# Kernel tuning notes

Measured on AMD Instinct MI355X. Metric: run time of the kernel, lower is better.

## Reference

```python
import jax, jax.numpy as jnp
import numpy as np

N, E, G = 100000, 1600000, 8
IN, H, OUT = 3, 64, 20


def setup_inputs() -> dict:
    key = jax.random.key(0)
    ks = jax.random.split(key, 24)
    def nrm(k, shape, scale=0.1):
        return jax.random.normal(k, shape, dtype=jnp.float32) * scale
    inp = {}
    inp["x"] = jax.random.normal(ks[0], (N, IN), dtype=jnp.float32)
    inp["edge_index"] = jax.random.randint(ks[1], (2, E), 0, N, dtype=jnp.int32)
    inp["batch"] = jnp.sort(jax.random.randint(ks[2], (N,), 0, G, dtype=jnp.int32))
    dims = [(IN, H), (H, H), (H, H)]  # 3 GATConv layers (initial + layers-1)
    for i, (di, do) in enumerate(dims):
        inp[f"W{i}"] = nrm(ks[3 + 4 * i], (di, do))
        inp[f"as{i}"] = nrm(ks[4 + 4 * i], (do,))
        inp[f"ad{i}"] = nrm(ks[5 + 4 * i], (do,))
        inp[f"b{i}"] = jnp.zeros((do,), jnp.float32)
    inp["vn_emb0"] = jnp.zeros((1, H), jnp.float32)  # constant-0 init per module
    inp["m1_w1"] = nrm(ks[15], (H, H)); inp["m1_b1"] = jnp.zeros((H,), jnp.float32)
    inp["m1_w2"] = nrm(ks[16], (H, H)); inp["m1_b2"] = jnp.zeros((H,), jnp.float32)
    inp["mf_w1"] = nrm(ks[17], (H, H)); inp["mf_b1"] = jnp.zeros((H,), jnp.float32)
    inp["mf_w2"] = nrm(ks[18], (H, OUT)); inp["mf_b2"] = jnp.zeros((OUT,), jnp.float32)
    inp["out_w"] = nrm(ks[19], (H, OUT)); inp["out_b"] = jnp.zeros((OUT,), jnp.float32)
    return inp


def _gat(x, src, dst, W, a_s, a_d, b):
    # PyG GATConv, 1 head: h = xW; e_ij = LeakyReLU_0.2(a_s.h_j + a_d.h_i);
    # alpha = softmax over incoming edges of each dst node; out_i = sum_j alpha_ij h_j + b
    h = x @ W                                                  # [N, H]
    lg = jax.nn.leaky_relu((h @ a_s)[src] + (h @ a_d)[dst], 0.2)  # [E+N]
    m = jax.ops.segment_max(lg, dst, num_segments=N)
    m = jnp.where(jnp.isfinite(m), m, 0.0)
    p = jnp.exp(lg - m[dst])
    denom = jax.ops.segment_sum(p, dst, num_segments=N)
    alpha = p / denom[dst]
    return jax.ops.segment_sum(alpha[:, None] * h[src], dst, num_segments=N) + b


def _forward(x, edge_index, batch, params):
    (W0, as0, ad0, b0, W1, as1, ad1, b1, W2, as2, ad2, b2,
     vn_emb0, m1_w1, m1_b1, m1_w2, m1_b2, mf_w1, mf_b1, mf_w2, mf_b2,
     out_w, out_b) = params
    loops = jnp.arange(N, dtype=edge_index.dtype)  # GATConv add_self_loops=True
    src = jnp.concatenate([edge_index[0], loops])
    dst = jnp.concatenate([edge_index[1], loops])
    act = lambda v: jax.nn.leaky_relu(v, 0.01)  # nn.LeakyReLU default slope
    h = act(_gat(x, src, dst, W0, as0, ad0, b0))
    h = act(_gat(h, src, dst, W1, as1, ad1, b1))
    h = act(_gat(h, src, dst, W2, as2, ad2, b2))
    # virtual node: global_add_pool(out, batch) + Embedding(0) (zero-init)
    vn = jax.ops.segment_sum(h, batch, num_segments=G) + vn_emb0[0]
    vn = jax.nn.relu(vn @ m1_w1 + m1_b1)
    vn = jax.nn.relu(vn @ m1_w2 + m1_b2)
    vn = jax.nn.relu(vn @ mf_w1 + mf_b1)
    vn = jax.nn.relu(vn @ mf_w2 + mf_b2)
    return (h @ out_w + out_b, vn)


def reference(x, edge_index, batch, W0, as0, ad0, b0, W1, as1, ad1, b1,
              W2, as2, ad2, b2, vn_emb0, m1_w1, m1_b1, m1_w2, m1_b2,
              mf_w1, mf_b1, mf_w2, mf_b2, out_w, out_b):
    params = (W0, as0, ad0, b0, W1, as1, ad1, b1, W2, as2, ad2, b2,
              vn_emb0, m1_w1, m1_b1, m1_w2, m1_b2, mf_w1, mf_b1, mf_w2, mf_b2,
              out_w, out_b)
    return _forward(x, edge_index, batch, params)
```

## Files before the change

### kernel.cpp

```cpp
#include <hip/hip_runtime.h>
#include <hip/hip_bf16.h>

#define H 64
#define OUTD 20
#define NGRAPH 8
#define CAP 64
#define NB 128

typedef __attribute__((ext_vector_type(8))) short bf16x8;
typedef __attribute__((ext_vector_type(4))) float f32x4;
typedef __attribute__((ext_vector_type(8))) unsigned short u16x8;

__device__ __forceinline__ float ldp(const void* p, int i, bool f32) {
    return f32 ? ((const float*)p)[i]
               : __bfloat162float(((const __hip_bfloat16*)p)[i]);
}

__device__ __forceinline__ float bfu(unsigned short u) {
    union { unsigned int i; float f; } c; c.i = ((unsigned)u) << 16; return c.f;
}
__device__ __forceinline__ unsigned short fbits(float f) {
    __hip_bfloat16 b = __float2bfloat16(f);
    return *reinterpret_cast<unsigned short*>(&b);
}

__global__ void detect_dtype(const unsigned short* __restrict__ xb, int n_u16,
                             int* __restrict__ flag) {
    __shared__ int sh[256];
    int t = threadIdx.x;
    int m = min(n_u16, 4096);
    int bad = 0;
    for (int i = t; i < m; i += 256) {
        unsigned e = (xb[i] >> 7) & 0xFF;
        bad += (e >= 0x90) ? 1 : 0;
    }
    sh[t] = bad;
    __syncthreads();
    for (int off = 128; off; off >>= 1) {
        if (t < off) sh[t] += sh[t + off];
        __syncthreads();
    }
    if (t == 0) *flag = (sh[0] > (m >> 4)) ? 1 : 0;
}


__global__ void bucketA_dense0(const int* __restrict__ dst, int* __restrict__ bcnt,
                               int E, int n, int nA, int EPC,
                               const void* __restrict__ x, const void* __restrict__ W,
                               const void* __restrict__ a_s, const void* __restrict__ a_d,
                               __hip_bfloat16* __restrict__ h, float* __restrict__ s,
                               float* __restrict__ d, const int* __restrict__ flagp) {
    if ((int)blockIdx.x < nA) {
        __shared__ unsigned acnt[NB];
        int t = threadIdx.x;
        for (int i = t; i < NB; i += 256) acnt[i] = 0;
        __syncthreads();
        int base = blockIdx.x * (256 * EPC) + t;
        for (int i = 0; i < EPC; ++i) {
            int e = base + i * 256;
            if (e < E) {
                int dn = dst[e];
                if ((unsigned)dn < (unsigned)n) atomicAdd(&acnt[dn >> 10], 1u);
            }
        }
        __syncthreads();
        for (int i = t; i < NB; i += 256) bcnt[blockIdx.x * NB + i] = acnt[i];
        return;
    }
    const bool f32 = (*flagp != 0);
    int idx = ((int)blockIdx.x - nA) * 256 + threadIdx.x;
    int node = idx >> 6;
    int f = idx & 63;
    if (node >= n) return;
    float acc = 0.f;
    for (int k = 0; k < 3; ++k)
        acc += ldp(x, node * 3 + k, f32) * ldp(W, k * H + f, f32);
    h[(size_t)node * H + f] = __float2bfloat16(acc);
    float sv = acc * ldp(a_s, f, f32);
    float dv = acc * ldp(a_d, f, f32);
    for (int off = 32; off; off >>= 1) {
        sv += __shfl_xor(sv, off);
        dv += __shfl_xor(dv, off);
    }
    if (f == 0) { s[node] = sv; d[node] = dv; }
}

__global__ void bucketB1(const int* __restrict__ bcnt, int* __restrict__ boff,
                         int* __restrict__ btot, int nA) {
    __shared__ int sh[256];
    int b = blockIdx.x, t = threadIdx.x;
    int v = (t < nA) ? bcnt[t * NB + b] : 0;
    sh[t] = v;
    __syncthreads();
    for (int off = 1; off < 256; off <<= 1) {
        int add = (t >= off) ? sh[t - off] : 0;
        __syncthreads();
        sh[t] += add;
        __syncthreads();
    }
    if (t < nA) boff[t * NB + b] = sh[t] - v;
    if (t == 255) btot[b] = sh[255];
}

__global__ void bucketB2(const int* __restrict__ btot, int* __restrict__ bstart) {
    __shared__ int sh[NB];
    int t = threadIdx.x;
    int v = btot[t];
    sh[t] = v;
    __syncthreads();
    for (int off = 1; off < NB; off <<= 1) {
        int add = (t >= off) ? sh[t - off] : 0;
        __syncthreads();
        sh[t] += add;
        __syncthreads();
    }
    bstart[t] = sh[t] - v;
    if (t == NB - 1) bstart[NB] = sh[NB - 1];
}

__global__ void bucketC(const int* __restrict__ src, const int* __restrict__ dst,
                        const int* __restrict__ boff, const int* __restrict__ bstart,
                        unsigned* __restrict__ ebuf, int E, int n, int EPC) {
    __shared__ int base[NB];
    __shared__ unsigned lcur[NB];
    int t = threadIdx.x;
    for (int i = t; i < NB; i += 256) {
        base[i] = bstart[i] + boff[blockIdx.x * NB + i];
        lcur[i] = 0;
    }
    __syncthreads();
    int eb = blockIdx.x * (256 * EPC) + t;
    for (int i = 0; i < EPC; ++i) {
        int e = eb + i * 256;
        if (e < E) {
            int dn = dst[e];
            if ((unsigned)dn < (unsigned)n) {
                int b = dn >> 10;
                unsigned pos = atomicAdd(&lcur[b], 1u);
                ebuf[base[b] + pos] = ((unsigned)src[e] << 10) | (unsigned)(dn & 1023);
            }
        }
    }
}

__global__ __launch_bounds__(1024) void bucketD(const unsigned* __restrict__ ebuf,
                                                const int* __restrict__ bstart,
                                                int* __restrict__ cnt,
                                                int* __restrict__ col, int n) {
    __shared__ unsigned lcnt[1024];
    int b = blockIdx.x, t = threadIdx.x;
    lcnt[t] = 0;
    __syncthreads();
    int beg = bstart[b], end = bstart[b + 1];
    for (int i = beg + t; i < end; i += 1024) {
        unsigned e = ebuf[i];
        int loc = (int)(e & 1023u);
        int sn = (int)(e >> 10);
        unsigned pos = atomicAdd(&lcnt[loc], 1u);
        if (pos < CAP) col[(size_t)((b << 10) + loc) * CAP + pos] = sn;
    }
    __syncthreads();
    int node = (b << 10) + t;
    if (node < n) cnt[node] = (int)min(lcnt[t], (unsigned)CAP);
}


__global__ __launch_bounds__(256) void denseN_mfma(
    const __hip_bfloat16* __restrict__ in,
    const void* __restrict__ W,
    const void* __restrict__ a_s, const void* __restrict__ a_d,
    __hip_bfloat16* __restrict__ h, float* __restrict__ s,
    float* __restrict__ d, int n, const int* __restrict__ flagp) {
    const bool f32 = (*flagp != 0);
    __shared__ short Wt[64 * 72];
    int t = threadIdx.x;
    for (int i = t; i < 4096; i += 256) {
        int k = i >> 6, nf = i & 63;
        Wt[nf * 72 + k] = (short)fbits(ldp(W, i, f32));
    }
    __syncthreads();

    int wid = t >> 6, lane = t & 63;
    int quad = lane >> 4, n16 = lane & 15;
    int nodeBase = blockIdx.x * 64 + wid * 16;
    int mrow = nodeBase + n16;
    int mclamp = min(mrow, n - 1);
    const short* inp = (const short*)in;
    const short* arow = inp + (size_t)mclamp * 64;
    bf16x8 a0 = *(const bf16x8*)(arow + quad * 8);
    bf16x8 a1 = *(const bf16x8*)(arow + 32 + quad * 8);

    float as_v[4], ad_v[4];
    for (int nt = 0; nt < 4; ++nt) {
        as_v[nt] = ldp(a_s, nt * 16 + n16, f32);
        ad_v[nt] = ldp(a_d, nt * 16 + n16, f32);
    }

    float sv[4] = {0.f, 0.f, 0.f, 0.f}, dv[4] = {0.f, 0.f, 0.f, 0.f};
    f32x4 accs[4];
    for (int nt = 0; nt < 4; ++nt) {
        const short* wrow = Wt + (nt * 16 + n16) * 72;
        bf16x8 b0 = *(const bf16x8*)(wrow + quad * 8);
        bf16x8 b1 = *(const bf16x8*)(wrow + 32 + quad * 8);
        f32x4 c = {0.f, 0.f, 0.f, 0.f};
        c = __builtin_amdgcn_mfma_f32_16x16x32_bf16(a0, b0, c, 0, 0, 0);
        c = __builtin_amdgcn_mfma_f32_16x16x32_bf16(a1, b1, c, 0, 0, 0);
        accs[nt] = c;
        for (int r = 0; r < 4; ++r) {
            sv[r] += c[r] * as_v[nt];
            dv[r] += c[r] * ad_v[nt];
        }
    }

    for (int r = 0; r < 4; ++r) {
        int node = nodeBase + quad * 4 + r;
        if (node < n) {
            __hip_bfloat16* hr = h + (size_t)node * 64;
            for (int nt = 0; nt < 4; ++nt)
                hr[nt * 16 + n16] = __float2bfloat16(accs[nt][r]);
        }
    }
    for (int r = 0; r < 4; ++r) {
        for (int mask = 1; mask < 16; mask <<= 1) {
            sv[r] += __shfl_xor(sv[r], mask);
            dv[r] += __shfl_xor(dv[r], mask);
        }
    }
    if (n16 == 0) {
        for (int r = 0; r < 4; ++r) {
            int node = nodeBase + quad * 4 + r;
            if (node < n) { s[node] = sv[r]; d[node] = dv[r]; }
        }
    }
}


__global__ void gat_aggregate(const __hip_bfloat16* __restrict__ h,
                              const float* __restrict__ s, const float* __restrict__ d,
                              const int* __restrict__ cnt, const int* __restrict__ col,
                              const void* __restrict__ bias,
                              __hip_bfloat16* __restrict__ out, int n,
                              const int* __restrict__ flagp) {
    const bool f32 = (*flagp != 0);
    int node = (blockIdx.x * blockDim.x + threadIdx.x) >> 6;
    if (node >= n) return;
    int lane = threadIdx.x & 63;
    int deg = min(cnt[node], CAP);
    int D = deg + 1;
    size_t base = (size_t)node * CAP;
    float di = d[node];

    if (D <= 64) {
        bool act = lane < D;
        int j = (lane < deg) ? col[base + lane] : node;
        j = ((unsigned)j < (unsigned)n) ? j : 0;
        float v = act ? s[j] + di : -INFINITY;
        v = v > 0.f ? v : 0.2f * v;
        float m = v;
        for (int off = 32; off; off >>= 1) m = fmaxf(m, __shfl_xor(m, off));
        float wgt = act ? __expf(v - m) : 0.f;
        float wsum = wgt;
        for (int off = 32; off; off >>= 1) wsum += __shfl_xor(wsum, off);

        const u16x8* h8 = (const u16x8*)h;
        int c = lane & 7, q = lane >> 3;
        float a[8] = {0.f, 0.f, 0.f, 0.f, 0.f, 0.f, 0.f, 0.f};
        int groups = (D + 7) >> 3;
        for (int p = 0; p < groups; ++p) {
            int t = 8 * p + q;
            float wt = __shfl(wgt, t);
            int jt = __shfl(j, t);
            u16x8 hv = h8[jt * 8 + c];
            a[0] += wt * bfu(hv[0]);
            a[1] += wt * bfu(hv[1]);
            a[2] += wt * bfu(hv[2]);
            a[3] += wt * bfu(hv[3]);
            a[4] += wt * bfu(hv[4]);
            a[5] += wt * bfu(hv[5]);
            a[6] += wt * bfu(hv[6]);
            a[7] += wt * bfu(hv[7]);
        }
        for (int i = 0; i < 8; ++i) {
            a[i] += __shfl_xor(a[i], 8);
            a[i] += __shfl_xor(a[i], 16);
            a[i] += __shfl_xor(a[i], 32);
        }
        if (lane < 8) {
            float inv = 1.f / fmaxf(wsum, 1e-20f);
            u16x8 ov;
            for (int i = 0; i < 8; ++i) {
                float o = a[i] * inv + ldp(bias, 8 * c + i, f32);
                o = o > 0.f ? o : 0.01f * o;
                ov[i] = fbits(o);
            }
            ((u16x8*)out)[(size_t)node * 8 + c] = ov;
        }
        return;
    }

    float m = -INFINITY;
    for (int e = lane; e < D; e += 64) {
        int j = (e < deg) ? col[base + e] : node;
        j = ((unsigned)j < (unsigned)n) ? j : 0;
        float v = s[j] + di;
        v = v > 0.f ? v : 0.2f * v;
        m = fmaxf(m, v);
    }
    for (int off = 32; off; off >>= 1) m = fmaxf(m, __shfl_xor(m, off));
    if (!(m > -INFINITY)) m = 0.f;

    float acc = 0.f, wsum = 0.f;
    for (int b = 0; b < D; b += 64) {
        int e = b + lane;
        float w = 0.f;
        int j = 0;
        if (e < D) {
            j = (e < deg) ? col[base + e] : node;
            j = ((unsigned)j < (unsigned)n) ? j : 0;
            float v = s[j] + di;
            v = v > 0.f ? v : 0.2f * v;
            w = __expf(v - m);
        }
        wsum += w;
        int c2 = min(64, D - b);
        for (int t = 0; t < c2; ++t) {
            float wt = __shfl(w, t);
            int jt = __shfl(j, t);
            acc += wt * __bfloat162float(h[(size_t)jt * H + lane]);
        }
    }
    for (int off = 32; off; off >>= 1) wsum += __shfl_xor(wsum, off);

    float o = acc / fmaxf(wsum, 1e-20f) + ldp(bias, lane, f32);
    o = o > 0.f ? o : 0.01f * o;
    out[(size_t)node * H + lane] = __float2bfloat16(o);
}


__global__ __launch_bounds__(256) void proj_pool(
    const __hip_bfloat16* __restrict__ h,
    const void* __restrict__ W, const void* __restrict__ b,
    void* __restrict__ out, int n, const int* __restrict__ flagp,
    int projBlocks, const int* __restrict__ batch, float* __restrict__ vn) {
    const bool f32 = (*flagp != 0);
    if ((int)blockIdx.x < projBlocks) {
        __shared__ short Wt[32 * 72];
        int t = threadIdx.x;
        for (int i = t; i < 32 * 64; i += 256) {
            int o = i >> 6, k = i & 63;
            Wt[o * 72 + k] = (o < OUTD) ? (short)fbits(ldp(W, k * OUTD + o, f32)) : 0;
        }
        __syncthreads();

        int wid = t >> 6, lane = t & 63;
        int quad = lane >> 4, n16 = lane & 15;
        int nodeBase = blockIdx.x * 64 + wid * 16;
        int mclamp = min(nodeBase + n16, n - 1);
        const short* arow = (const short*)h + (size_t)mclamp * 64;
        bf16x8 a0 = *(const bf16x8*)(arow + quad * 8);
        bf16x8 a1 = *(const bf16x8*)(arow + 32 + quad * 8);

        f32x4 acc0 = {0.f, 0.f, 0.f, 0.f}, acc1 = {0.f, 0.f, 0.f, 0.f};
        {
            const short* wrow = Wt + n16 * 72;
            bf16x8 b0 = *(const bf16x8*)(wrow + quad * 8);
            bf16x8 b1 = *(const bf16x8*)(wrow + 32 + quad * 8);
            acc0 = __builtin_amdgcn_mfma_f32_16x16x32_bf16(a0, b0, acc0, 0, 0, 0);
            acc0 = __builtin_amdgcn_mfma_f32_16x16x32_bf16(a1, b1, acc0, 0, 0, 0);
        }
        {
            const short* wrow = Wt + (16 + n16) * 72;
            bf16x8 b0 = *(const bf16x8*)(wrow + quad * 8);
            bf16x8 b1 = *(const bf16x8*)(wrow + 32 + quad * 8);
            acc1 = __builtin_amdgcn_mfma_f32_16x16x32_bf16(a0, b0, acc1, 0, 0, 0);
            acc1 = __builtin_amdgcn_mfma_f32_16x16x32_bf16(a1, b1, acc1, 0, 0, 0);
        }
        float bv0 = ldp(b, n16, f32);
        float bv1 = (n16 < OUTD - 16) ? ldp(b, 16 + n16, f32) : 0.f;
        for (int r = 0; r < 4; ++r) {
            int node = nodeBase + quad * 4 + r;
            if (node >= n) break;
            float o0 = acc0[r] + bv0;
            if (f32) ((float*)out)[node * OUTD + n16] = o0;
            else     ((__hip_bfloat16*)out)[node * OUTD + n16] = __float2bfloat16(o0);
            if (n16 < OUTD - 16) {
                float o1 = acc1[r] + bv1;
                if (f32) ((float*)out)[node * OUTD + 16 + n16] = o1;
                else     ((__hip_bfloat16*)out)[node * OUTD + 16 + n16] = __float2bfloat16(o1);
            }
        }
        return;
    }
    __shared__ float part[NGRAPH * H];
    int t = threadIdx.x;
    for (int i = t; i < NGRAPH * H; i += 256) part[i] = 0.f;
    __syncthreads();
    int pb = (int)blockIdx.x - projBlocks;
    int npb = gridDim.x - projBlocks;
    int wid = t >> 6, lane = t & 63;
    int gwave = pb * 4 + wid;
    int nwaves = npb * 4;
    int chunk = (n + nwaves - 1) / nwaves;
    int beg = gwave * chunk;
    int end = min(n, beg + chunk);
    if (beg < end) {
        float acc = 0.f;
        int cur = batch[beg];
        for (int i = beg; i < end; ++i) {
            int g = batch[i];
            if (g != cur) {
                if ((unsigned)cur < NGRAPH) atomicAdd(&part[cur * H + lane], acc);
                acc = 0.f;
                cur = g;
            }
            acc += __bfloat162float(h[(size_t)i * H + lane]);
        }
        if ((unsigned)cur < NGRAPH) atomicAdd(&part[cur * H + lane], acc);
    }
    __syncthreads();
    for (int i = t; i < NGRAPH * H; i += 256) {
        float v = part[i];
        if (v != 0.f) atomicAdd(&vn[i], v);
    }
}


__global__ void vn_mlp(const float* __restrict__ vn, const void* __restrict__ emb,
                       const void* __restrict__ w1, const void* __restrict__ b1,
                       const void* __restrict__ w2, const void* __restrict__ b2,
                       const void* __restrict__ w3, const void* __restrict__ b3,
                       const void* __restrict__ w4, const void* __restrict__ b4,
                       void* __restrict__ out, int out1_off, const int* __restrict__ flagp) {
    const bool f32 = (*flagp != 0);
    __shared__ float A[NGRAPH * H], B[NGRAPH * H];
    int t = threadIdx.x;
    int g = t >> 6, f = t & 63;
    A[t] = vn[t] + ldp(emb, f, f32);
    __syncthreads();
    float acc = ldp(b1, f, f32);
    for (int k = 0; k < H; ++k) acc += A[g * H + k] * ldp(w1, k * H + f, f32);
    B[t] = fmaxf(acc, 0.f);
    __syncthreads();
    acc = ldp(b2, f, f32);
    for (int k = 0; k < H; ++k) acc += B[g * H + k] * ldp(w2, k * H + f, f32);
    A[t] = fmaxf(acc, 0.f);
    __syncthreads();
    acc = ldp(b3, f, f32);
    for (int k = 0; k < H; ++k) acc += A[g * H + k] * ldp(w3, k * H + f, f32);
    B[t] = fmaxf(acc, 0.f);
    __syncthreads();
    if (f < OUTD) {
        acc = ldp(b4, f, f32);
        for (int k = 0; k < H; ++k) acc += B[g * H + k] * ldp(w4, k * OUTD + f, f32);
        acc = fmaxf(acc, 0.f);
        int idx = out1_off + g * OUTD + f;
        if (f32) ((float*)out)[idx] = acc;
        else     ((__hip_bfloat16*)out)[idx] = __float2bfloat16(acc);
    }
}


extern "C" void kernel_launch(void* const* d_in, const int* in_sizes, int n_in,
                              void* d_out, int out_size, void* d_ws, size_t ws_size,
                              hipStream_t stream) {
    const void* x   = d_in[0];
    const int* ei   = (const int*)d_in[1];
    const int* batch= (const int*)d_in[2];
    const void* W0  = d_in[3];
    const void* as0 = d_in[4];
    const void* ad0 = d_in[5];
    const void* b0  = d_in[6];
    const void* W1  = d_in[7];
    const void* as1 = d_in[8];
    const void* ad1 = d_in[9];
    const void* b1  = d_in[10];
    const void* W2  = d_in[11];
    const void* as2 = d_in[12];
    const void* ad2 = d_in[13];
    const void* b2  = d_in[14];
    const void* vne = d_in[15];
    const void* m1w1 = d_in[16];
    const void* m1b1 = d_in[17];
    const void* m1w2 = d_in[18];
    const void* m1b2 = d_in[19];
    const void* mfw1 = d_in[20];
    const void* mfb1 = d_in[21];
    const void* mfw2 = d_in[22];
    const void* mfb2 = d_in[23];
    const void* outw = d_in[24];
    const void* outb = d_in[25];

    const int N = in_sizes[2];
    const int E = in_sizes[1] / 2;
    const int* srcp = ei;
    const int* dstp = ei + E;

    char* w = (char*)d_ws;
    auto alloc = [&](size_t bytes) -> void* {
        void* p = (void*)w;
        w += ((bytes + 255) / 256) * 256;
        return p;
    };
    int*   flag   = (int*)alloc(256);
    int*   bcnt   = (int*)alloc((size_t)256 * NB * 4);
    int*   boff   = (int*)alloc((size_t)256 * NB * 4);
    int*   btot   = (int*)alloc((size_t)NB * 4);
    int*   bstart = (int*)alloc((size_t)(NB + 1) * 4);
    unsigned* ebuf= (unsigned*)alloc((size_t)E * 4);
    int*   cnt    = (int*)alloc((size_t)N * 4);
    int*   col    = (int*)alloc((size_t)N * CAP * 4);
    __hip_bfloat16* featA = (__hip_bfloat16*)alloc((size_t)N * H * 2);
    __hip_bfloat16* featB = (__hip_bfloat16*)alloc((size_t)N * H * 2);
    __hip_bfloat16* hbuf  = (__hip_bfloat16*)alloc((size_t)N * H * 2);
    float* sArr   = (float*)alloc((size_t)N * 4);
    float* dArr   = (float*)alloc((size_t)N * 4);
    float* vn     = (float*)alloc((size_t)NGRAPH * H * 4);

    const int nbN64 = (N * H + 255) / 256;
    const int nb64 = (N + 63) / 64;
    const int projBlocks = (N + 63) / 64;
    int EPC = 32;
    int nA = (E + 256 * EPC - 1) / (256 * EPC);
    while (nA > 256) { EPC <<= 1; nA = (E + 256 * EPC - 1) / (256 * EPC); }

    detect_dtype<<<1, 256, 0, stream>>>((const unsigned short*)x, in_sizes[0], flag);

    hipMemsetAsync(vn, 0, (size_t)NGRAPH * H * 4, stream);
    bucketA_dense0<<<nA + nbN64, 256, 0, stream>>>(
        dstp, bcnt, E, N, nA, EPC, x, W0, as0, ad0, hbuf, sArr, dArr, flag);
    bucketB1<<<NB, 256, 0, stream>>>(bcnt, boff, btot, nA);
    bucketB2<<<1, NB, 0, stream>>>(btot, bstart);
    bucketC<<<nA, 256, 0, stream>>>(srcp, dstp, boff, bstart, ebuf, E, N, EPC);
    bucketD<<<NB, 1024, 0, stream>>>(ebuf, bstart, cnt, col, N);

    gat_aggregate<<<nbN64, 256, 0, stream>>>(hbuf, sArr, dArr, cnt, col, b0, featA, N, flag);
    denseN_mfma<<<nb64, 256, 0, stream>>>(featA, W1, as1, ad1, hbuf, sArr, dArr, N, flag);
    gat_aggregate<<<nbN64, 256, 0, stream>>>(hbuf, sArr, dArr, cnt, col, b1, featB, N, flag);
    denseN_mfma<<<nb64, 256, 0, stream>>>(featB, W2, as2, ad2, hbuf, sArr, dArr, N, flag);
    gat_aggregate<<<nbN64, 256, 0, stream>>>(hbuf, sArr, dArr, cnt, col, b2, featA, N, flag);

    proj_pool<<<projBlocks + 512, 256, 0, stream>>>(featA, outw, outb, d_out, N, flag,
                                                    projBlocks, batch, vn);
    vn_mlp<<<1, 512, 0, stream>>>(vn, vne, m1w1, m1b1, m1w2, m1b2, mfw1, mfb1, mfw2, mfb2,
                                  d_out, N * OUTD, flag);
}
```

Measured before the change: 440.0 us.

## Fuse GAT aggregation with next-layer dense projection and final proj/pool

Each GAT layer's neighbor aggregation now writes its 64 node rows into LDS, and the same block then runs the MFMA projection for the next layer, or the output projection plus graph pooling for the last layer. This removes the global write and re-read of the intermediate feature arrays and cuts three kernel launches. The h/s/d buffers are ping-ponged because aggregation reads neighbors' values while new ones are written. The trade-offs are more LDS per block, and fewer, longer blocks (64 nodes each, 16 sequential nodes per wave), which may reduce latency hiding for the gather-heavy aggregation. Pooling now does LDS atomics from every block instead of a separate dedicated group of pooling blocks.

```diff
diff --git a/kernel.cpp b/kernel.cpp
--- a/kernel.cpp
+++ b/kernel.cpp
@@ -165,14 +165,122 @@
 }
 
 
-__global__ __launch_bounds__(256) void denseN_mfma(
-    const __hip_bfloat16* __restrict__ in,
+__device__ __forceinline__ void gat_node_to_lds(
+    int node, int lane, const __hip_bfloat16* __restrict__ h,
+    const float* __restrict__ s, const float* __restrict__ d,
+    const int* __restrict__ cnt, const int* __restrict__ col,
+    const void* __restrict__ bias, bool f32, int n, short* Rrow) {
+    if (node >= n) {
+        if (lane < 8) {
+            u16x8 zz; for (int i = 0; i < 8; ++i) zz[i] = 0;
+            *(u16x8*)(Rrow + lane * 8) = zz;
+        }
+        return;
+    }
+    int deg = min(cnt[node], CAP);
+    int D = deg + 1;
+    size_t base = (size_t)node * CAP;
+    float di = d[node];
+
+    if (D <= 64) {
+        bool act = lane < D;
+        int j = (lane < deg) ? col[base + lane] : node;
+        j = ((unsigned)j < (unsigned)n) ? j : 0;
+        float v = act ? s[j] + di : -INFINITY;
+        v = v > 0.f ? v : 0.2f * v;
+        float m = v;
+        for (int off = 32; off; off >>= 1) m = fmaxf(m, __shfl_xor(m, off));
+        float wgt = act ? __expf(v - m) : 0.f;
+        float wsum = wgt;
+        for (int off = 32; off; off >>= 1) wsum += __shfl_xor(wsum, off);
+
+        const u16x8* h8 = (const u16x8*)h;
+        int c = lane & 7, q = lane >> 3;
+        float a[8] = {0.f, 0.f, 0.f, 0.f, 0.f, 0.f, 0.f, 0.f};
+        int groups = (D + 7) >> 3;
+        for (int p = 0; p < groups; ++p) {
+            int tt = 8 * p + q;
+            float wt = __shfl(wgt, tt);
+            int jt = __shfl(j, tt);
+            u16x8 hv = h8[jt * 8 + c];
+            a[0] += wt * bfu(hv[0]);
+            a[1] += wt * bfu(hv[1]);
+            a[2] += wt * bfu(hv[2]);
+            a[3] += wt * bfu(hv[3]);
+            a[4] += wt * bfu(hv[4]);
+            a[5] += wt * bfu(hv[5]);
+            a[6] += wt * bfu(hv[6]);
+            a[7] += wt * bfu(hv[7]);
+        }
+        for (int i = 0; i < 8; ++i) {
+            a[i] += __shfl_xor(a[i], 8);
+            a[i] += __shfl_xor(a[i], 16);
+            a[i] += __shfl_xor(a[i], 32);
+        }
+        if (lane < 8) {
+            float inv = 1.f / fmaxf(wsum, 1e-20f);
+            u16x8 ov;
+            for (int i = 0; i < 8; ++i) {
+                float o = a[i] * inv + ldp(bias, 8 * c + i, f32);
+                o = o > 0.f ? o : 0.01f * o;
+                ov[i] = fbits(o);
+            }
+            *(u16x8*)(Rrow + c * 8) = ov;
+        }
+        return;
+    }
+
+    float m = -INFINITY;
+    for (int e = lane; e < D; e += 64) {
+        int j = (e < deg) ? col[base + e] : node;
+        j = ((unsigned)j < (unsigned)n) ? j : 0;
+        float v = s[j] + di;
+        v = v > 0.f ? v : 0.2f * v;
+        m = fmaxf(m, v);
+    }
+    for (int off = 32; off; off >>= 1) m = fmaxf(m, __shfl_xor(m, off));
+    if (!(m > -INFINITY)) m = 0.f;
+
+    float acc = 0.f, wsum = 0.f;
+    for (int b = 0; b < D; b += 64) {
+        int e = b + lane;
+        float w = 0.f;
+        int j = 0;
+        if (e < D) {
+            j = (e < deg) ? col[base + e] : node;
+            j = ((unsigned)j < (unsigned)n) ? j : 0;
+            float v = s[j] + di;
+            v = v > 0.f ? v : 0.2f * v;
+            w = __expf(v - m);
+        }
+        wsum += w;
+        int c2 = min(64, D - b);
+        for (int tt = 0; tt < c2; ++tt) {
+            float wt = __shfl(w, tt);
+            int jt = __shfl(j, tt);
+            acc += wt * __bfloat162float(h[(size_t)jt * H + lane]);
+        }
+    }
+    for (int off = 32; off; off >>= 1) wsum += __shfl_xor(wsum, off);
+
+    float o = acc / fmaxf(wsum, 1e-20f) + ldp(bias, lane, f32);
+    o = o > 0.f ? o : 0.01f * o;
+    Rrow[lane] = (short)fbits(o);
+}
+
+
+__global__ __launch_bounds__(256) void gat_dense(
+    const __hip_bfloat16* __restrict__ h,
+    const float* __restrict__ s, const float* __restrict__ d,
+    const int* __restrict__ cnt, const int* __restrict__ col,
+    const void* __restrict__ bias,
     const void* __restrict__ W,
     const void* __restrict__ a_s, const void* __restrict__ a_d,
-    __hip_bfloat16* __restrict__ h, float* __restrict__ s,
-    float* __restrict__ d, int n, const int* __restrict__ flagp) {
+    __hip_bfloat16* __restrict__ hout, float* __restrict__ sout,
+    float* __restrict__ dout, int n, const int* __restrict__ flagp) {
     const bool f32 = (*flagp != 0);
     __shared__ short Wt[64 * 72];
+    __shared__ short R[64 * 72];
     int t = threadIdx.x;
     for (int i = t; i < 4096; i += 256) {
         int k = i >> 6, nf = i & 63;
@@ -181,12 +289,17 @@
     __syncthreads();
 
     int wid = t >> 6, lane = t & 63;
+    int blockBase = blockIdx.x * 64;
+    short* Rw = R + (wid * 16) * 72;
+
+    for (int it = 0; it < 16; ++it)
+        gat_node_to_lds(blockBase + wid * 16 + it, lane, h, s, d, cnt, col,
+                        bias, f32, n, Rw + it * 72);
+    __syncthreads();
+
     int quad = lane >> 4, n16 = lane & 15;
-    int nodeBase = blockIdx.x * 64 + wid * 16;
-    int mrow = nodeBase + n16;
-    int mclamp = min(mrow, n - 1);
-    const short* inp = (const short*)in;
-    const short* arow = inp + (size_t)mclamp * 64;
+    int nodeBase = blockBase + wid * 16;
+    const short* arow = R + (size_t)(wid * 16 + n16) * 72;
     bf16x8 a0 = *(const bf16x8*)(arow + quad * 8);
     bf16x8 a1 = *(const bf16x8*)(arow + 32 + quad * 8);
 
@@ -215,7 +328,7 @@
     for (int r = 0; r < 4; ++r) {
         int node = nodeBase + quad * 4 + r;
         if (node < n) {
-            __hip_bfloat16* hr = h + (size_t)node * 64;
+            __hip_bfloat16* hr = hout + (size_t)node * 64;
             for (int nt = 0; nt < 4; ++nt)
                 hr[nt * 16 + n16] = __float2bfloat16(accs[nt][r]);
         }
@@ -229,194 +342,91 @@
     if (n16 == 0) {
         for (int r = 0; r < 4; ++r) {
             int node = nodeBase + quad * 4 + r;
-            if (node < n) { s[node] = sv[r]; d[node] = dv[r]; }
-        }
-    }
-}
-
-
-__global__ void gat_aggregate(const __hip_bfloat16* __restrict__ h,
-                              const float* __restrict__ s, const float* __restrict__ d,
-                              const int* __restrict__ cnt, const int* __restrict__ col,
-                              const void* __restrict__ bias,
-                              __hip_bfloat16* __restrict__ out, int n,
-                              const int* __restrict__ flagp) {
+            if (node < n) { sout[node] = sv[r]; dout[node] = dv[r]; }
+        }
+    }
+}
+
+
+__global__ __launch_bounds__(256) void gat_proj_pool(
+    const __hip_bfloat16* __restrict__ h,
+    const float* __restrict__ s, const float* __restrict__ d,
+    const int* __restrict__ cnt, const int* __restrict__ col,
+    const void* __restrict__ bias,
+    const void* __restrict__ Wp, const void* __restrict__ bp,
+    void* __restrict__ out, const int* __restrict__ batch,
+    float* __restrict__ vn, int n, const int* __restrict__ flagp) {
     const bool f32 = (*flagp != 0);
-    int node = (blockIdx.x * blockDim.x + threadIdx.x) >> 6;
-    if (node >= n) return;
-    int lane = threadIdx.x & 63;
-    int deg = min(cnt[node], CAP);
-    int D = deg + 1;
-    size_t base = (size_t)node * CAP;
-    float di = d[node];
-
-    if (D <= 64) {
-        bool act = lane < D;
-        int j = (lane < deg) ? col[base + lane] : node;
-        j = ((unsigned)j < (unsigned)n) ? j : 0;
-        float v = act ? s[j] + di : -INFINITY;
-        v = v > 0.f ? v : 0.2f * v;
-        float m = v;
-        for (int off = 32; off; off >>= 1) m = fmaxf(m, __shfl_xor(m, off));
-        float wgt = act ? __expf(v - m) : 0.f;
-        float wsum = wgt;
-        for (int off = 32; off; off >>= 1) wsum += __shfl_xor(wsum, off);
-
-        const u16x8* h8 = (const u16x8*)h;
-        int c = lane & 7, q = lane >> 3;
-        float a[8] = {0.f, 0.f, 0.f, 0.f, 0.f, 0.f, 0.f, 0.f};
-        int groups = (D + 7) >> 3;
-        for (int p = 0; p < groups; ++p) {
-            int t = 8 * p + q;
-            float wt = __shfl(wgt, t);
-            int jt = __shfl(j, t);
-            u16x8 hv = h8[jt * 8 + c];
-            a[0] += wt * bfu(hv[0]);
-            a[1] += wt * bfu(hv[1]);
-            a[2] += wt * bfu(hv[2]);
-            a[3] += wt * bfu(hv[3]);
-            a[4] += wt * bfu(hv[4]);
-            a[5] += wt * bfu(hv[5]);
-            a[6] += wt * bfu(hv[6]);
-            a[7] += wt * bfu(hv[7]);
-        }
-        for (int i = 0; i < 8; ++i) {
-            a[i] += __shfl_xor(a[i], 8);
-            a[i] += __shfl_xor(a[i], 16);
-            a[i] += __shfl_xor(a[i], 32);
-        }
-        if (lane < 8) {
-            float inv = 1.f / fmaxf(wsum, 1e-20f);
-            u16x8 ov;
-            for (int i = 0; i < 8; ++i) {
-                float o = a[i] * inv + ldp(bias, 8 * c + i, f32);
-                o = o > 0.f ? o : 0.01f * o;
-                ov[i] = fbits(o);
-            }
-            ((u16x8*)out)[(size_t)node * 8 + c] = ov;
-        }
-        return;
-    }
-
-    float m = -INFINITY;
-    for (int e = lane; e < D; e += 64) {
-        int j = (e < deg) ? col[base + e] : node;
-        j = ((unsigned)j < (unsigned)n) ? j : 0;
-        float v = s[j] + di;
-        v = v > 0.f ? v : 0.2f * v;
-        m = fmaxf(m, v);
-    }
-    for (int off = 32; off; off >>= 1) m = fmaxf(m, __shfl_xor(m, off));
-    if (!(m > -INFINITY)) m = 0.f;
-
-    float acc = 0.f, wsum = 0.f;
-    for (int b = 0; b < D; b += 64) {
-        int e = b + lane;
-        float w = 0.f;
-        int j = 0;
-        if (e < D) {
-            j = (e < deg) ? col[base + e] : node;
-            j = ((unsigned)j < (unsigned)n) ? j : 0;
-            float v = s[j] + di;
-            v = v > 0.f ? v : 0.2f * v;
-            w = __expf(v - m);
-        }
-        wsum += w;
-        int c2 = min(64, D - b);
-        for (int t = 0; t < c2; ++t) {
-            float wt = __shfl(w, t);
-            int jt = __shfl(j, t);
-            acc += wt * __bfloat162float(h[(size_t)jt * H + lane]);
-        }
-    }
-    for (int off = 32; off; off >>= 1) wsum += __shfl_xor(wsum, off);
-
-    float o = acc / fmaxf(wsum, 1e-20f) + ldp(bias, lane, f32);
-    o = o > 0.f ? o : 0.01f * o;
-    out[(size_t)node * H + lane] = __float2bfloat16(o);
-}
-
-
-__global__ __launch_bounds__(256) void proj_pool(
-    const __hip_bfloat16* __restrict__ h,
-    const void* __restrict__ W, const void* __restrict__ b,
-    void* __restrict__ out, int n, const int* __restrict__ flagp,
-    int projBlocks, const int* __restrict__ batch, float* __restrict__ vn) {
-    const bool f32 = (*flagp != 0);
-    if ((int)blockIdx.x < projBlocks) {
-        __shared__ short Wt[32 * 72];
-        int t = threadIdx.x;
-        for (int i = t; i < 32 * 64; i += 256) {
-            int o = i >> 6, k = i & 63;
-            Wt[o * 72 + k] = (o < OUTD) ? (short)fbits(ldp(W, k * OUTD + o, f32)) : 0;
-        }
-        __syncthreads();
-
-        int wid = t >> 6, lane = t & 63;
-        int quad = lane >> 4, n16 = lane & 15;
-        int nodeBase = blockIdx.x * 64 + wid * 16;
-        int mclamp = min(nodeBase + n16, n - 1);
-        const short* arow = (const short*)h + (size_t)mclamp * 64;
-        bf16x8 a0 = *(const bf16x8*)(arow + quad * 8);
-        bf16x8 a1 = *(const bf16x8*)(arow + 32 + quad * 8);
-
-        f32x4 acc0 = {0.f, 0.f, 0.f, 0.f}, acc1 = {0.f, 0.f, 0.f, 0.f};
-        {
-            const short* wrow = Wt + n16 * 72;
-            bf16x8 b0 = *(const bf16x8*)(wrow + quad * 8);
-            bf16x8 b1 = *(const bf16x8*)(wrow + 32 + quad * 8);
-            acc0 = __builtin_amdgcn_mfma_f32_16x16x32_bf16(a0, b0, acc0, 0, 0, 0);
-            acc0 = __builtin_amdgcn_mfma_f32_16x16x32_bf16(a1, b1, acc0, 0, 0, 0);
-        }
-        {
-            const short* wrow = Wt + (16 + n16) * 72;
-            bf16x8 b0 = *(const bf16x8*)(wrow + quad * 8);
-            bf16x8 b1 = *(const bf16x8*)(wrow + 32 + quad * 8);
-            acc1 = __builtin_amdgcn_mfma_f32_16x16x32_bf16(a0, b0, acc1, 0, 0, 0);
-            acc1 = __builtin_amdgcn_mfma_f32_16x16x32_bf16(a1, b1, acc1, 0, 0, 0);
-        }
-        float bv0 = ldp(b, n16, f32);
-        float bv1 = (n16 < OUTD - 16) ? ldp(b, 16 + n16, f32) : 0.f;
-        for (int r = 0; r < 4; ++r) {
-            int node = nodeBase + quad * 4 + r;
-            if (node >= n) break;
-            float o0 = acc0[r] + bv0;
-            if (f32) ((float*)out)[node * OUTD + n16] = o0;
-            else     ((__hip_bfloat16*)out)[node * OUTD + n16] = __float2bfloat16(o0);
-            if (n16 < OUTD - 16) {
-                float o1 = acc1[r] + bv1;
-                if (f32) ((float*)out)[node * OUTD + 16 + n16] = o1;
-                else     ((__hip_bfloat16*)out)[node * OUTD + 16 + n16] = __float2bfloat16(o1);
-            }
-        }
-        return;
-    }
+    __shared__ short Wt[32 * 72];
+    __shared__ short R[64 * 72];
     __shared__ float part[NGRAPH * H];
     int t = threadIdx.x;
+    for (int i = t; i < 32 * 64; i += 256) {
+        int o = i >> 6, k = i & 63;
+        Wt[o * 72 + k] = (o < OUTD) ? (short)fbits(ldp(Wp, k * OUTD + o, f32)) : 0;
+    }
     for (int i = t; i < NGRAPH * H; i += 256) part[i] = 0.f;
     __syncthreads();
-    int pb = (int)blockIdx.x - projBlocks;
-    int npb = gridDim.x - projBlocks;
+
     int wid = t >> 6, lane = t & 63;
-    int gwave = pb * 4 + wid;
-    int nwaves = npb * 4;
-    int chunk = (n + nwaves - 1) / nwaves;
-    int beg = gwave * chunk;
-    int end = min(n, beg + chunk);
-    if (beg < end) {
-        float acc = 0.f;
-        int cur = batch[beg];
-        for (int i = beg; i < end; ++i) {
-            int g = batch[i];
-            if (g != cur) {
-                if ((unsigned)cur < NGRAPH) atomicAdd(&part[cur * H + lane], acc);
-                acc = 0.f;
-                cur = g;
-            }
-            acc += __bfloat162float(h[(size_t)i * H + lane]);
-        }
-        if ((unsigned)cur < NGRAPH) atomicAdd(&part[cur * H + lane], acc);
-    }
+    int blockBase = blockIdx.x * 64;
+    short* Rw = R + (wid * 16) * 72;
+
+    for (int it = 0; it < 16; ++it)
+        gat_node_to_lds(blockBase + wid * 16 + it, lane, h, s, d, cnt, col,
+                        bias, f32, n, Rw + it * 72);
+    __syncthreads();
+
+    int quad = lane >> 4, n16 = lane & 15;
+    int nodeBase = blockBase + wid * 16;
+    const short* arow = R + (size_t)(wid * 16 + n16) * 72;
+    bf16x8 a0 = *(const bf16x8*)(arow + quad * 8);
+    bf16x8 a1 = *(const bf16x8*)(arow + 32 + quad * 8);
+
+    f32x4 acc0 = {0.f, 0.f, 0.f, 0.f}, acc1 = {0.f, 0.f, 0.f, 0.f};
+    {
+        const short* wrow = Wt + n16 * 72;
+        bf16x8 b0 = *(const bf16x8*)(wrow + quad * 8);
+        bf16x8 b1 = *(const bf16x8*)(wrow + 32 + quad * 8);
+        acc0 = __builtin_amdgcn_mfma_f32_16x16x32_bf16(a0, b0, acc0, 0, 0, 0);
+        acc0 = __builtin_amdgcn_mfma_f32_16x16x32_bf16(a1, b1, acc0, 0, 0, 0);
+    }
+    {
+        const short* wrow = Wt + (16 + n16) * 72;
+        bf16x8 b0 = *(const bf16x8*)(wrow + quad * 8);
+        bf16x8 b1 = *(const bf16x8*)(wrow + 32 + quad * 8);
+        acc1 = __builtin_amdgcn_mfma_f32_16x16x32_bf16(a0, b0, acc1, 0, 0, 0);
+        acc1 = __builtin_amdgcn_mfma_f32_16x16x32_bf16(a1, b1, acc1, 0, 0, 0);
+    }
+    float bv0 = ldp(bp, n16, f32);
+    float bv1 = (n16 < OUTD - 16) ? ldp(bp, 16 + n16, f32) : 0.f;
+    for (int r = 0; r < 4; ++r) {
+        int node = nodeBase + quad * 4 + r;
+        if (node >= n) break;
+        float o0 = acc0[r] + bv0;
+        if (f32) ((float*)out)[node * OUTD + n16] = o0;
+        else     ((__hip_bfloat16*)out)[node * OUTD + n16] = __float2bfloat16(o0);
+        if (n16 < OUTD - 16) {
+            float o1 = acc1[r] + bv1;
+            if (f32) ((float*)out)[node * OUTD + 16 + n16] = o1;
+            else     ((__hip_bfloat16*)out)[node * OUTD + 16 + n16] = __float2bfloat16(o1);
+        }
+    }
+
+    float acc = 0.f;
+    int cur = -1;
+    for (int it = 0; it < 16; ++it) {
+        int node = blockBase + wid * 16 + it;
+        if (node >= n) break;
+        int g = batch[node];
+        if (g != cur) {
+            if ((unsigned)cur < NGRAPH) atomicAdd(&part[cur * H + lane], acc);
+            acc = 0.f;
+            cur = g;
+        }
+        acc += bfu((unsigned short)Rw[it * 72 + lane]);
+    }
+    if ((unsigned)cur < NGRAPH) atomicAdd(&part[cur * H + lane], acc);
     __syncthreads();
     for (int i = t; i < NGRAPH * H; i += 256) {
         float v = part[i];
@@ -509,16 +519,16 @@
     unsigned* ebuf= (unsigned*)alloc((size_t)E * 4);
     int*   cnt    = (int*)alloc((size_t)N * 4);
     int*   col    = (int*)alloc((size_t)N * CAP * 4);
-    __hip_bfloat16* featA = (__hip_bfloat16*)alloc((size_t)N * H * 2);
-    __hip_bfloat16* featB = (__hip_bfloat16*)alloc((size_t)N * H * 2);
-    __hip_bfloat16* hbuf  = (__hip_bfloat16*)alloc((size_t)N * H * 2);
-    float* sArr   = (float*)alloc((size_t)N * 4);
-    float* dArr   = (float*)alloc((size_t)N * 4);
+    __hip_bfloat16* hA = (__hip_bfloat16*)alloc((size_t)N * H * 2);
+    __hip_bfloat16* hB = (__hip_bfloat16*)alloc((size_t)N * H * 2);
+    float* sA     = (float*)alloc((size_t)N * 4);
+    float* dA     = (float*)alloc((size_t)N * 4);
+    float* sB     = (float*)alloc((size_t)N * 4);
+    float* dB     = (float*)alloc((size_t)N * 4);
     float* vn     = (float*)alloc((size_t)NGRAPH * H * 4);
 
     const int nbN64 = (N * H + 255) / 256;
     const int nb64 = (N + 63) / 64;
-    const int projBlocks = (N + 63) / 64;
     int EPC = 32;
     int nA = (E + 256 * EPC - 1) / (256 * EPC);
     while (nA > 256) { EPC <<= 1; nA = (E + 256 * EPC - 1) / (256 * EPC); }
@@ -527,20 +537,18 @@
 
     hipMemsetAsync(vn, 0, (size_t)NGRAPH * H * 4, stream);
     bucketA_dense0<<<nA + nbN64, 256, 0, stream>>>(
-        dstp, bcnt, E, N, nA, EPC, x, W0, as0, ad0, hbuf, sArr, dArr, flag);
+        dstp, bcnt, E, N, nA, EPC, x, W0, as0, ad0, hA, sA, dA, flag);
     bucketB1<<<NB, 256, 0, stream>>>(bcnt, boff, btot, nA);
     bucketB2<<<1, NB, 0, stream>>>(btot, bstart);
     bucketC<<<nA, 256, 0, stream>>>(srcp, dstp, boff, bstart, ebuf, E, N, EPC);
     bucketD<<<NB, 1024, 0, stream>>>(ebuf, bstart, cnt, col, N);
 
-    gat_aggregate<<<nbN64, 256, 0, stream>>>(hbuf, sArr, dArr, cnt, col, b0, featA, N, flag);
-    denseN_mfma<<<nb64, 256, 0, stream>>>(featA, W1, as1, ad1, hbuf, sArr, dArr, N, flag);
-    gat_aggregate<<<nbN64, 256, 0, stream>>>(hbuf, sArr, dArr, cnt, col, b1, featB, N, flag);
-    denseN_mfma<<<nb64, 256, 0, stream>>>(featB, W2, as2, ad2, hbuf, sArr, dArr, N, flag);
-    gat_aggregate<<<nbN64, 256, 0, stream>>>(hbuf, sArr, dArr, cnt, col, b2, featA, N, flag);
-
-    proj_pool<<<projBlocks + 512, 256, 0, stream>>>(featA, outw, outb, d_out, N, flag,
-                                                    projBlocks, batch, vn);
+    gat_dense<<<nb64, 256, 0, stream>>>(hA, sA, dA, cnt, col, b0,
+                                        W1, as1, ad1, hB, sB, dB, N, flag);
+    gat_dense<<<nb64, 256, 0, stream>>>(hB, sB, dB, cnt, col, b1,
+                                        W2, as2, ad2, hA, sA, dA, N, flag);
+    gat_proj_pool<<<nb64, 256, 0, stream>>>(hA, sA, dA, cnt, col, b2,
+                                            outw, outb, d_out, batch, vn, N, flag);
     vn_mlp<<<1, 512, 0, stream>>>(vn, vne, m1w1, m1b1, m1w2, m1b2, mfw1, mfb1, mfw2, mfb2,
                                   d_out, N * OUTD, flag);
 }
```

New measurement: 538.4 us. +22.4%, slower.
